# Performance work log

Hardware: AMD Instinct MI355X
Metric: run time of the kernel (lower is better)

The kernel has to match this reference:

```python
import jax, jax.numpy as jnp
import numpy as np

N_NODES = 50000
N_EDGES = 640000
HIDDEN = 128
NUM_CONVS = 3
VOCAB = 100  # nn.Embedding(100, hidden_dim)


def setup_inputs() -> dict:
    key = jax.random.key(0)
    ks = jax.random.split(key, 8)
    z = jax.random.randint(ks[0], (N_NODES,), 0, VOCAB)
    edge_index = jax.random.randint(ks[1], (2, N_EDGES), 0, N_NODES)
    edge_attr = jax.random.normal(ks[2], (N_EDGES, HIDDEN), jnp.float32)
    emb = jax.random.normal(ks[3], (VOCAB, HIDDEN), jnp.float32) * 0.02
    s = 1.0 / np.sqrt(HIDDEN)
    # Stacked per-conv MLP params: Linear(H,H) -> relu -> Linear(H,H)
    W1 = jax.random.uniform(ks[4], (NUM_CONVS, HIDDEN, HIDDEN), jnp.float32, -s, s)
    b1 = jnp.zeros((NUM_CONVS, HIDDEN), jnp.float32)
    W2 = jax.random.uniform(ks[5], (NUM_CONVS, HIDDEN, HIDDEN), jnp.float32, -s, s)
    b2 = jnp.zeros((NUM_CONVS, HIDDEN), jnp.float32)
    return dict(z=z, edge_index=edge_index, edge_attr=edge_attr,
                emb=emb, W1=W1, b1=b1, W2=W2, b2=b2)


def reference(z, edge_index, edge_attr, emb, W1, b1, W2, b2):
    x = emb[z]  # [N, H] node embeddings
    src, dst = edge_index[0], edge_index[1]
    n = x.shape[0]
    num_convs = W1.shape[0]
    for i in range(num_convs):
        # GINEConv: message = relu(x_j + edge_attr), aggr='add' at dst
        msg = jax.nn.relu(x[src] + edge_attr)                      # [E, H]
        agg = jax.ops.segment_sum(msg, dst, num_segments=n)        # [N, H]
        out = agg + x  # (1 + eps) * x_r with eps = 0
        # MultiLayerPerceptron(H, [H, H], activation='relu'): relu between layers only
        h = jax.nn.relu(out @ W1[i] + b1[i]) @ W2[i] + b2[i]
        if i < num_convs - 1:
            h = jax.nn.relu(h)  # inter-conv activation
        x = h + x  # short_cut residual
    return x  # concat_hidden=False -> last hidden
```

## Files before the change

### kernel.cpp

```cpp
#include <hip/hip_runtime.h>

#define HID 128
#define NNODE 50000
#define NEDGE 640000

typedef __attribute__((ext_vector_type(8))) short bf16x8;
typedef __attribute__((ext_vector_type(4))) float f32x4;

static __global__ void embed_kernel(const int* __restrict__ z,
                                    const float* __restrict__ emb,
                                    float* __restrict__ x) {
  int i = blockIdx.x * 256 + threadIdx.x;
  const int total = NNODE * (HID / 4);
  if (i >= total) return;
  int node = i >> 5;
  int c = i & 31;
  ((float4*)x)[i] = ((const float4*)emb)[(size_t)z[node] * 32 + c];
}

static __global__ void hist_kernel(const int* __restrict__ dst, int* __restrict__ deg) {
  int i = blockIdx.x * 256 + threadIdx.x;
  if (i < NEDGE) atomicAdd(&deg[dst[i]], 1);
}

static __global__ void scan_kernel(const int* __restrict__ deg,
                                   int* __restrict__ row_ptr,
                                   int* __restrict__ cursor) {
  __shared__ int sums[1024];
  int t = threadIdx.x;
  const int per = (NNODE + 1023) / 1024;
  int base = t * per;
  int s = 0;
  for (int i = 0; i < per; ++i) {
    int idx = base + i;
    if (idx < NNODE) s += deg[idx];
  }
  sums[t] = s;
  __syncthreads();
  for (int off = 1; off < 1024; off <<= 1) {
    int v = (t >= off) ? sums[t - off] : 0;
    __syncthreads();
    if (t >= off) sums[t] += v;
    __syncthreads();
  }
  int run = (t == 0) ? 0 : sums[t - 1];
  for (int i = 0; i < per; ++i) {
    int idx = base + i;
    if (idx < NNODE) {
      row_ptr[idx] = run;
      cursor[idx] = run;
      run += deg[idx];
    }
  }
  if (t == 1023) row_ptr[NNODE] = run;
}

static __global__ void fill_kernel(const int* __restrict__ src, const int* __restrict__ dst,
                                   int* __restrict__ cursor, int2* __restrict__ elist) {
  int i = blockIdx.x * 256 + threadIdx.x;
  if (i < NEDGE) {
    int d = dst[i];
    int p = atomicAdd(&cursor[d], 1);
    elist[p] = make_int2(i, src[i]);
  }
}

static __global__ void wsplit_kernel(const float* __restrict__ W1, const float* __restrict__ W2,
                                     unsigned short* __restrict__ whi,
                                     unsigned short* __restrict__ wlo) {
  int idx = blockIdx.x * 256 + threadIdx.x;
  if (idx >= 6 * 16384) return;
  int cg = idx >> 14;
  int rem = idx & 16383;
  int k = rem >> 7, n = rem & 127;
  int c = cg >> 1, g = cg & 1;
  float v = (g ? W2 : W1)[c * 16384 + k * 128 + n];
  unsigned u = __float_as_uint(v);
  unsigned hb = u >> 16;
  float hf = __uint_as_float(hb << 16);
  unsigned lb = __float_as_uint(v - hf) >> 16;
  int o = cg * 17408 + n * 136 + k;
  whi[o] = (unsigned short)hb;
  wlo[o] = (unsigned short)lb;
}

static __global__ __launch_bounds__(256) void gather_kernel(
    const float* __restrict__ x, const float* __restrict__ ea,
    const int* __restrict__ row_ptr, const int2* __restrict__ elist,
    float* __restrict__ out) {
  int wave = threadIdx.x >> 6;
  int lane = threadIdx.x & 63;
  int node = blockIdx.x * 4 + wave;
  if (node >= NNODE) return;
  const float2* x2 = (const float2*)x;
  const double* ed = (const double*)ea;
  float2 a0 = x2[(size_t)node * 64 + lane];
  float2 a1 = make_float2(0.f, 0.f);
  float2 a2 = make_float2(0.f, 0.f);
  float2 a3 = make_float2(0.f, 0.f);
  int j  = row_ptr[node];
  int je = row_ptr[node + 1];
  for (; j + 4 <= je; j += 4) {
    int2 e0 = elist[j], e1 = elist[j + 1], e2i = elist[j + 2], e3 = elist[j + 3];
    float2 xv0 = x2[(size_t)e0.y * 64 + lane];
    double d0 = __builtin_nontemporal_load(&ed[(size_t)e0.x * 64 + lane]);
    float2 xv1 = x2[(size_t)e1.y * 64 + lane];
    double d1 = __builtin_nontemporal_load(&ed[(size_t)e1.x * 64 + lane]);
    float2 xv2 = x2[(size_t)e2i.y * 64 + lane];
    double d2 = __builtin_nontemporal_load(&ed[(size_t)e2i.x * 64 + lane]);
    float2 xv3 = x2[(size_t)e3.y * 64 + lane];
    double d3 = __builtin_nontemporal_load(&ed[(size_t)e3.x * 64 + lane]);
    float2 ev0 = *(float2*)&d0, ev1 = *(float2*)&d1;
    float2 ev2 = *(float2*)&d2, ev3 = *(float2*)&d3;
    a0.x += fmaxf(xv0.x + ev0.x, 0.f); a0.y += fmaxf(xv0.y + ev0.y, 0.f);
    a1.x += fmaxf(xv1.x + ev1.x, 0.f); a1.y += fmaxf(xv1.y + ev1.y, 0.f);
    a2.x += fmaxf(xv2.x + ev2.x, 0.f); a2.y += fmaxf(xv2.y + ev2.y, 0.f);
    a3.x += fmaxf(xv3.x + ev3.x, 0.f); a3.y += fmaxf(xv3.y + ev3.y, 0.f);
  }
  for (; j < je; ++j) {
    int2 es = elist[j];
    float2 xv = x2[(size_t)es.y * 64 + lane];
    double d0 = __builtin_nontemporal_load(&ed[(size_t)es.x * 64 + lane]);
    float2 ev = *(float2*)&d0;
    a0.x += fmaxf(xv.x + ev.x, 0.f);
    a0.y += fmaxf(xv.y + ev.y, 0.f);
  }
  a0.x += a1.x + a2.x + a3.x;
  a0.y += a1.y + a2.y + a3.y;
  ((float2*)out)[(size_t)node * 64 + lane] = a0;
}

static __global__ __launch_bounds__(256) void mlp_mfma(
    const float* __restrict__ in, const float* __restrict__ xres,
    const unsigned short* __restrict__ wt1hi, const unsigned short* __restrict__ wt1lo,
    const unsigned short* __restrict__ wt2hi, const unsigned short* __restrict__ wt2lo,
    const float* __restrict__ b1, const float* __restrict__ b2,
    float* __restrict__ xout, int relu_out) {
  __shared__ unsigned short WbHi[128 * 72];
  __shared__ unsigned short WbLo[128 * 72];
  __shared__ float Ts[64 * 132];
  const int tid = threadIdx.x;
  const int w = tid >> 6, l = tid & 63;
  const int lm = l & 15, quad = l >> 4;
  const int row0 = blockIdx.x * 64;

  float b1v[8], b2v[8];
#pragma unroll
  for (int t = 0; t < 8; ++t) { b1v[t] = b1[t * 16 + lm]; b2v[t] = b2[t * 16 + lm]; }

  f32x4 acc[8];
#pragma unroll
  for (int t = 0; t < 8; ++t) acc[t] = (f32x4){0.f, 0.f, 0.f, 0.f};

  int arow = row0 + w * 16 + lm;
  if (arow >= NNODE) arow = NNODE - 1;

  for (int kc = 0; kc < 128; kc += 64) {
    __syncthreads();
    for (int idx = tid; idx < 128 * 8; idx += 256) {
      int n = idx >> 3, seg = idx & 7;
      *(uint4*)&WbHi[n * 72 + seg * 8] = *(const uint4*)&wt1hi[n * 136 + kc + seg * 8];
      *(uint4*)&WbLo[n * 72 + seg * 8] = *(const uint4*)&wt1lo[n * 136 + kc + seg * 8];
    }
    __syncthreads();
#pragma unroll
    for (int ks = 0; ks < 64; ks += 32) {
      const float* ap = in + (size_t)arow * 128 + kc + ks + quad * 8;
      float4 av0 = *(const float4*)ap;
      float4 av1 = *(const float4*)(ap + 4);
      float av[8] = {av0.x, av0.y, av0.z, av0.w, av1.x, av1.y, av1.z, av1.w};
      bf16x8 ah, al;
#pragma unroll
      for (int jj = 0; jj < 8; ++jj) {
        unsigned u = __float_as_uint(av[jj]);
        unsigned hb = u >> 16;
        float hf = __uint_as_float(hb << 16);
        unsigned lb = __float_as_uint(av[jj] - hf) >> 16;
        ah[jj] = (short)hb; al[jj] = (short)lb;
      }
#pragma unroll
      for (int t = 0; t < 8; ++t) {
        int off = (t * 16 + lm) * 72 + ks + quad * 8;
        bf16x8 bh = *(const bf16x8*)&WbHi[off];
        bf16x8 bl = *(const bf16x8*)&WbLo[off];
        acc[t] = __builtin_amdgcn_mfma_f32_16x16x32_bf16(ah, bh, acc[t], 0, 0, 0);
        acc[t] = __builtin_amdgcn_mfma_f32_16x16x32_bf16(ah, bl, acc[t], 0, 0, 0);
        acc[t] = __builtin_amdgcn_mfma_f32_16x16x32_bf16(al, bh, acc[t], 0, 0, 0);
      }
    }
  }
  __syncthreads();

#pragma unroll
  for (int t = 0; t < 8; ++t)
#pragma unroll
    for (int r = 0; r < 4; ++r)
      Ts[(w * 16 + quad * 4 + r) * 132 + t * 16 + lm] = fmaxf(acc[t][r] + b1v[t], 0.f);

#pragma unroll
  for (int t = 0; t < 8; ++t) acc[t] = (f32x4){0.f, 0.f, 0.f, 0.f};
  __syncthreads();

  for (int kc = 0; kc < 128; kc += 64) {
    __syncthreads();
    for (int idx = tid; idx < 128 * 8; idx += 256) {
      int n = idx >> 3, seg = idx & 7;
      *(uint4*)&WbHi[n * 72 + seg * 8] = *(const uint4*)&wt2hi[n * 136 + kc + seg * 8];
      *(uint4*)&WbLo[n * 72 + seg * 8] = *(const uint4*)&wt2lo[n * 136 + kc + seg * 8];
    }
    __syncthreads();
#pragma unroll
    for (int ks = 0; ks < 64; ks += 32) {
      const float* tp = &Ts[(w * 16 + lm) * 132 + kc + ks + quad * 8];
      float4 av0 = *(const float4*)tp;
      float4 av1 = *(const float4*)(tp + 4);
      float av[8] = {av0.x, av0.y, av0.z, av0.w, av1.x, av1.y, av1.z, av1.w};
      bf16x8 ah, al;
#pragma unroll
      for (int jj = 0; jj < 8; ++jj) {
        unsigned u = __float_as_uint(av[jj]);
        unsigned hb = u >> 16;
        float hf = __uint_as_float(hb << 16);
        unsigned lb = __float_as_uint(av[jj] - hf) >> 16;
        ah[jj] = (short)hb; al[jj] = (short)lb;
      }
#pragma unroll
      for (int t = 0; t < 8; ++t) {
        int off = (t * 16 + lm) * 72 + ks + quad * 8;
        bf16x8 bh = *(const bf16x8*)&WbHi[off];
        bf16x8 bl = *(const bf16x8*)&WbLo[off];
        acc[t] = __builtin_amdgcn_mfma_f32_16x16x32_bf16(ah, bh, acc[t], 0, 0, 0);
        acc[t] = __builtin_amdgcn_mfma_f32_16x16x32_bf16(ah, bl, acc[t], 0, 0, 0);
        acc[t] = __builtin_amdgcn_mfma_f32_16x16x32_bf16(al, bh, acc[t], 0, 0, 0);
      }
    }
  }

#pragma unroll
  for (int t = 0; t < 8; ++t) {
#pragma unroll
    for (int r = 0; r < 4; ++r) {
      int row = row0 + w * 16 + quad * 4 + r;
      if (row < NNODE) {
        int col = t * 16 + lm;
        float v = acc[t][r] + b2v[t];
        if (relu_out) v = fmaxf(v, 0.f);
        v += xres[(size_t)row * 128 + col];
        xout[(size_t)row * 128 + col] = v;
      }
    }
  }
}

extern "C" void kernel_launch(void* const* d_in, const int* in_sizes, int n_in,
                              void* d_out, int out_size, void* d_ws, size_t ws_size,
                              hipStream_t stream) {
  const int*   z   = (const int*)d_in[0];
  const int*   ei  = (const int*)d_in[1];
  const float* ea  = (const float*)d_in[2];
  const float* emb = (const float*)d_in[3];
  const float* W1  = (const float*)d_in[4];
  const float* b1  = (const float*)d_in[5];
  const float* W2  = (const float*)d_in[6];
  const float* b2  = (const float*)d_in[7];
  float* outp = (float*)d_out;

  char* ws = (char*)d_ws;
  float* xbuf   = (float*)(ws + 0);
  float* obuf   = (float*)(ws + 25600000);
  int*   deg    = (int*)  (ws + 51200000);
  int*   cursor = (int*)  (ws + 51400000);
  int*   rowptr = (int*)  (ws + 51600000);
  int2*  elist  = (int2*) (ws + 51800016);
  unsigned short* whi = (unsigned short*)(ws + 57000000);
  unsigned short* wlo = (unsigned short*)(ws + 57250000);

  const int* srcv = ei;
  const int* dstv = ei + NEDGE;

  hipMemsetAsync(deg, 0, NNODE * sizeof(int), stream);
  embed_kernel<<<(NNODE * 32 + 255) / 256, 256, 0, stream>>>(z, emb, xbuf);
  hist_kernel<<<(NEDGE + 255) / 256, 256, 0, stream>>>(dstv, deg);
  scan_kernel<<<1, 1024, 0, stream>>>(deg, rowptr, cursor);
  fill_kernel<<<(NEDGE + 255) / 256, 256, 0, stream>>>(srcv, dstv, cursor, elist);
  wsplit_kernel<<<(6 * 16384 + 255) / 256, 256, 0, stream>>>(W1, W2, whi, wlo);

  for (int i = 0; i < 3; ++i) {
    gather_kernel<<<(NNODE + 3) / 4, 256, 0, stream>>>(xbuf, ea, rowptr, elist, obuf);
    float* xo = (i == 2) ? outp : xbuf;
    mlp_mfma<<<(NNODE + 63) / 64, 256, 0, stream>>>(
        obuf, xbuf,
        whi + (size_t)(i * 2 + 0) * 17408, wlo + (size_t)(i * 2 + 0) * 17408,
        whi + (size_t)(i * 2 + 1) * 17408, wlo + (size_t)(i * 2 + 1) * 17408,
        b1 + (size_t)i * HID, b2 + (size_t)i * HID,
        xo, (i < 2) ? 1 : 0);
  }
}
```

Measured before the change: 967.5 us.

## Permute edge_attr into CSR order once and stream it contiguously in gathers

Adds a one-time permute kernel that copies edge_attr rows into destination-sorted CSR order and extracts a separate source-index array. Each of the three gather passes then reads edge features sequentially instead of via random row indices, and the unroll goes from 4 to 8 edges. The intent is to make the dominant edge_attr traffic contiguous and to raise memory-level parallelism. The cost is an extra full read and write of the 327 MB edge_attr tensor, plus about 330 MB more workspace.

```diff
diff --git a/kernel.cpp b/kernel.cpp
--- a/kernel.cpp
+++ b/kernel.cpp
@@ -63,6 +63,79 @@
     int p = atomicAdd(&cursor[d], 1);
     elist[p] = make_int2(i, src[i]);
   }
+}
+
+static __global__ void permute_kernel(const float* __restrict__ ea,
+                                      const int2* __restrict__ elist,
+                                      int* __restrict__ srcp,
+                                      float* __restrict__ eap) {
+  int t = blockIdx.x * 256 + threadIdx.x;
+  const int total = NEDGE * 32;
+  if (t >= total) return;
+  int j = t >> 5, seg = t & 31;
+  int2 es = elist[j];
+  float4 v = ((const float4*)ea)[(size_t)es.x * 32 + seg];
+  ((float4*)eap)[(size_t)j * 32 + seg] = v;
+  if (seg == 0) srcp[j] = es.y;
+}
+
+static __global__ __launch_bounds__(256) void gather_kernel(
+    const float* __restrict__ x, const float* __restrict__ eap,
+    const int* __restrict__ row_ptr, const int* __restrict__ srcp,
+    float* __restrict__ out) {
+  int wave = threadIdx.x >> 6;
+  int lane = threadIdx.x & 63;
+  int node = blockIdx.x * 4 + wave;
+  if (node >= NNODE) return;
+  const float2* x2 = (const float2*)x;
+  const double* ed = (const double*)eap;
+  float2 a0 = x2[(size_t)node * 64 + lane];
+  float2 a1 = make_float2(0.f, 0.f);
+  float2 a2 = make_float2(0.f, 0.f);
+  float2 a3 = make_float2(0.f, 0.f);
+  int j  = row_ptr[node];
+  int je = row_ptr[node + 1];
+  for (; j + 8 <= je; j += 8) {
+    double d0 = __builtin_nontemporal_load(&ed[(size_t)(j + 0) * 64 + lane]);
+    double d1 = __builtin_nontemporal_load(&ed[(size_t)(j + 1) * 64 + lane]);
+    double d2 = __builtin_nontemporal_load(&ed[(size_t)(j + 2) * 64 + lane]);
+    double d3 = __builtin_nontemporal_load(&ed[(size_t)(j + 3) * 64 + lane]);
+    double d4 = __builtin_nontemporal_load(&ed[(size_t)(j + 4) * 64 + lane]);
+    double d5 = __builtin_nontemporal_load(&ed[(size_t)(j + 5) * 64 + lane]);
+    double d6 = __builtin_nontemporal_load(&ed[(size_t)(j + 6) * 64 + lane]);
+    double d7 = __builtin_nontemporal_load(&ed[(size_t)(j + 7) * 64 + lane]);
+    int s0 = srcp[j + 0], s1 = srcp[j + 1], s2 = srcp[j + 2], s3 = srcp[j + 3];
+    int s4 = srcp[j + 4], s5 = srcp[j + 5], s6 = srcp[j + 6], s7 = srcp[j + 7];
+    float2 xv0 = x2[(size_t)s0 * 64 + lane];
+    float2 xv1 = x2[(size_t)s1 * 64 + lane];
+    float2 xv2 = x2[(size_t)s2 * 64 + lane];
+    float2 xv3 = x2[(size_t)s3 * 64 + lane];
+    float2 xv4 = x2[(size_t)s4 * 64 + lane];
+    float2 xv5 = x2[(size_t)s5 * 64 + lane];
+    float2 xv6 = x2[(size_t)s6 * 64 + lane];
+    float2 xv7 = x2[(size_t)s7 * 64 + lane];
+    float2 e0 = *(float2*)&d0, e1 = *(float2*)&d1, e2 = *(float2*)&d2, e3 = *(float2*)&d3;
+    float2 e4 = *(float2*)&d4, e5 = *(float2*)&d5, e6 = *(float2*)&d6, e7 = *(float2*)&d7;
+    a0.x += fmaxf(xv0.x + e0.x, 0.f); a0.y += fmaxf(xv0.y + e0.y, 0.f);
+    a1.x += fmaxf(xv1.x + e1.x, 0.f); a1.y += fmaxf(xv1.y + e1.y, 0.f);
+    a2.x += fmaxf(xv2.x + e2.x, 0.f); a2.y += fmaxf(xv2.y + e2.y, 0.f);
+    a3.x += fmaxf(xv3.x + e3.x, 0.f); a3.y += fmaxf(xv3.y + e3.y, 0.f);
+    a0.x += fmaxf(xv4.x + e4.x, 0.f); a0.y += fmaxf(xv4.y + e4.y, 0.f);
+    a1.x += fmaxf(xv5.x + e5.x, 0.f); a1.y += fmaxf(xv5.y + e5.y, 0.f);
+    a2.x += fmaxf(xv6.x + e6.x, 0.f); a2.y += fmaxf(xv6.y + e6.y, 0.f);
+    a3.x += fmaxf(xv7.x + e7.x, 0.f); a3.y += fmaxf(xv7.y + e7.y, 0.f);
+  }
+  for (; j < je; ++j) {
+    double d0 = __builtin_nontemporal_load(&ed[(size_t)j * 64 + lane]);
+    int s0 = srcp[j];
+    float2 xv = x2[(size_t)s0 * 64 + lane];
+    float2 ev = *(float2*)&d0;
+    a0.x += fmaxf(xv.x + ev.x, 0.f);
+    a0.y += fmaxf(xv.y + ev.y, 0.f);
+  }
+  a0.x += a1.x + a2.x + a3.x;
+  a0.y += a1.y + a2.y + a3.y;
+  ((float2*)out)[(size_t)node * 64 + lane] = a0;
 }
 
 static __global__ void wsplit_kernel(const float* __restrict__ W1, const float* __restrict__ W2,
@@ -84,52 +157,6 @@
   wlo[o] = (unsigned short)lb;
 }
 
-static __global__ __launch_bounds__(256) void gather_kernel(
-    const float* __restrict__ x, const float* __restrict__ ea,
-    const int* __restrict__ row_ptr, const int2* __restrict__ elist,
-    float* __restrict__ out) {
-  int wave = threadIdx.x >> 6;
-  int lane = threadIdx.x & 63;
-  int node = blockIdx.x * 4 + wave;
-  if (node >= NNODE) return;
-  const float2* x2 = (const float2*)x;
-  const double* ed = (const double*)ea;
-  float2 a0 = x2[(size_t)node * 64 + lane];
-  float2 a1 = make_float2(0.f, 0.f);
-  float2 a2 = make_float2(0.f, 0.f);
-  float2 a3 = make_float2(0.f, 0.f);
-  int j  = row_ptr[node];
-  int je = row_ptr[node + 1];
-  for (; j + 4 <= je; j += 4) {
-    int2 e0 = elist[j], e1 = elist[j + 1], e2i = elist[j + 2], e3 = elist[j + 3];
-    float2 xv0 = x2[(size_t)e0.y * 64 + lane];
-    double d0 = __builtin_nontemporal_load(&ed[(size_t)e0.x * 64 + lane]);
-    float2 xv1 = x2[(size_t)e1.y * 64 + lane];
-    double d1 = __builtin_nontemporal_load(&ed[(size_t)e1.x * 64 + lane]);
-    float2 xv2 = x2[(size_t)e2i.y * 64 + lane];
-    double d2 = __builtin_nontemporal_load(&ed[(size_t)e2i.x * 64 + lane]);
-    float2 xv3 = x2[(size_t)e3.y * 64 + lane];
-    double d3 = __builtin_nontemporal_load(&ed[(size_t)e3.x * 64 + lane]);
-    float2 ev0 = *(float2*)&d0, ev1 = *(float2*)&d1;
-    float2 ev2 = *(float2*)&d2, ev3 = *(float2*)&d3;
-    a0.x += fmaxf(xv0.x + ev0.x, 0.f); a0.y += fmaxf(xv0.y + ev0.y, 0.f);
-    a1.x += fmaxf(xv1.x + ev1.x, 0.f); a1.y += fmaxf(xv1.y + ev1.y, 0.f);
-    a2.x += fmaxf(xv2.x + ev2.x, 0.f); a2.y += fmaxf(xv2.y + ev2.y, 0.f);
-    a3.x += fmaxf(xv3.x + ev3.x, 0.f); a3.y += fmaxf(xv3.y + ev3.y, 0.f);
-  }
-  for (; j < je; ++j) {
-    int2 es = elist[j];
-    float2 xv = x2[(size_t)es.y * 64 + lane];
-    double d0 = __builtin_nontemporal_load(&ed[(size_t)es.x * 64 + lane]);
-    float2 ev = *(float2*)&d0;
-    a0.x += fmaxf(xv.x + ev.x, 0.f);
-    a0.y += fmaxf(xv.y + ev.y, 0.f);
-  }
-  a0.x += a1.x + a2.x + a3.x;
-  a0.y += a1.y + a2.y + a3.y;
-  ((float2*)out)[(size_t)node * 64 + lane] = a0;
-}
-
 static __global__ __launch_bounds__(256) void mlp_mfma(
     const float* __restrict__ in, const float* __restrict__ xres,
     const unsigned short* __restrict__ wt1hi, const unsigned short* __restrict__ wt1lo,
@@ -274,6 +301,8 @@
   int2*  elist  = (int2*) (ws + 51800016);
   unsigned short* whi = (unsigned short*)(ws + 57000000);
   unsigned short* wlo = (unsigned short*)(ws + 57250000);
+  int*   srcp   = (int*)  (ws + 57500000);
+  float* eaperm = (float*)(ws + 60100000);
 
   const int* srcv = ei;
   const int* dstv = ei + NEDGE;
@@ -283,10 +312,11 @@
   hist_kernel<<<(NEDGE + 255) / 256, 256, 0, stream>>>(dstv, deg);
   scan_kernel<<<1, 1024, 0, stream>>>(deg, rowptr, cursor);
   fill_kernel<<<(NEDGE + 255) / 256, 256, 0, stream>>>(srcv, dstv, cursor, elist);
+  permute_kernel<<<(NEDGE * 32) / 256, 256, 0, stream>>>(ea, elist, srcp, eaperm);
   wsplit_kernel<<<(6 * 16384 + 255) / 256, 256, 0, stream>>>(W1, W2, whi, wlo);
 
   for (int i = 0; i < 3; ++i) {
-    gather_kernel<<<(NNODE + 3) / 4, 256, 0, stream>>>(xbuf, ea, rowptr, elist, obuf);
+    gather_kernel<<<(NNODE + 3) / 4, 256, 0, stream>>>(xbuf, eaperm, rowptr, srcp, obuf);
     float* xo = (i == 2) ? outp : xbuf;
     mlp_mfma<<<(NNODE + 63) / 64, 256, 0, stream>>>(
         obuf, xbuf,
```

After: 1.165 ms. +20.4%, slower.
